# Performance work log

Measured on AMD Instinct MI355X. Metric: run time of the kernel, lower is better.

The kernel has to match this reference:

```python
import jax, jax.numpy as jnp
import numpy as np

N_NODES = 100000
N_EDGES = 1600000
D_IN = 128
D_OUT = 64
NUM_LAYERS = 3
BN_EPS = 1e-5


def setup_inputs() -> dict:
    key = jax.random.key(0)
    k_x, k_e, k_w = jax.random.split(key, 3)
    x = jax.random.normal(k_x, (N_NODES, D_IN), dtype=jnp.float32)
    edge_index = jax.random.randint(k_e, (2, N_EDGES), 0, N_NODES, dtype=jnp.int64)
    bn_gamma = jnp.ones((NUM_LAYERS, D_IN), dtype=jnp.float32)
    bn_beta = jnp.zeros((NUM_LAYERS, D_IN), dtype=jnp.float32)
    W = jax.random.normal(k_w, (D_IN, D_OUT), dtype=jnp.float32) * (1.0 / np.sqrt(D_IN))
    b = jnp.zeros((D_OUT,), dtype=jnp.float32)
    return {"x": x, "edge_index": edge_index, "bn_gamma": bn_gamma, "bn_beta": bn_beta, "W": W, "b": b}


def reference(x, edge_index, bn_gamma, bn_beta, W, b):
    # GNN forward, task='node', aggregate='sum', combine='sum', readout='sum',
    # recursive_weighting=False, training mode (no sigmoid, BN uses batch stats).
    n = x.shape[0]
    dst = edge_index[0]  # spmm(Adj, h): pooled[i] = sum over edges (i <- j) of h[j]
    src = edge_index[1]
    h = x
    for layer in range(NUM_LAYERS):
        # neighbor aggregate: sparse spmm == gather + segment-sum scatter
        agg = jax.ops.segment_sum(h[src], dst, num_segments=n)  # [N, D]
        # graph readout (single batched graph): sum over nodes, broadcast to every node
        readout = jnp.sum(h, axis=0, keepdims=True)  # [1, D]
        # functional 'sum' combine of (self, aggregated, readout)
        h = h + agg + readout
        # BatchNorm1d over the node dimension (training statistics, biased var)
        mean = jnp.mean(h, axis=0)
        var = jnp.var(h, axis=0)
        h = (h - mean) * jax.lax.rsqrt(var + BN_EPS) * bn_gamma[layer] + bn_beta[layer]
        h = jax.nn.relu(h)
    # node-task head (training branch: raw logits)
    return h @ W + b
```

## Files before the change

kernel.cpp:

```cpp
#include <hip/hip_runtime.h>

#define D 128
#define DOUT 64
#define BN_EPS 1e-5f
#define BCAP 96
#define SCAP 224

typedef unsigned int   u32;
typedef unsigned short u16;
typedef short  short8 __attribute__((ext_vector_type(8)));
typedef float  f32x4  __attribute__((ext_vector_type(4)));

__device__ __forceinline__ u16 f2bf(float f) {
    u32 x = __float_as_uint(f);
    x += 0x7fffu + ((x >> 16) & 1u);
    return (u16)(x >> 16);
}
__device__ __forceinline__ float bflo(u32 u) { return __uint_as_float(u << 16); }
__device__ __forceinline__ float bfhi(u32 u) { return __uint_as_float(u & 0xffff0000u); }

__global__ void init_kernel(const float* __restrict__ x, u16* __restrict__ xb,
                            int* __restrict__ bcnt,
                            float* __restrict__ stats,
                            const float* __restrict__ W, u16* __restrict__ wt,
                            int n_nodes, int n_ctr) {
    int total = n_nodes * (D / 4);
    for (int t = blockIdx.x * blockDim.x + threadIdx.x; t < total;
         t += gridDim.x * blockDim.x) {
        float4 v = ((const float4*)x)[t];
        ((ushort4*)xb)[t] = make_ushort4(f2bf(v.x), f2bf(v.y), f2bf(v.z), f2bf(v.w));
        if (t < n_ctr) bcnt[t] = 0;
        if (t < 2048) stats[t] = (t >= 256 && t < 384) ? 1.f : 0.f;
        if (t < D * DOUT) {
            int c = t >> 7, k = t & (D - 1);
            wt[t] = f2bf(W[k * DOUT + c]);
        }
    }
}

__global__ void partA_kernel(const int* __restrict__ ei, int* __restrict__ bcnt,
                             uint2* __restrict__ pairs, int n_edges) {
    int slot = blockIdx.x & 7;
    for (int e = blockIdx.x * blockDim.x + threadIdx.x; e < n_edges;
         e += gridDim.x * blockDim.x) {
        int d = ei[e];
        int s = ei[n_edges + e];
        int sb = ((d >> 6) << 3) + slot;
        int pos = atomicAdd(&bcnt[sb << 4], 1);
        if (pos < SCAP) pairs[(size_t)sb * SCAP + pos] = make_uint2((u32)d, (u32)s);
    }
}

__global__ void partB_kernel(const uint2* __restrict__ pairs,
                             const int* __restrict__ bcnt,
                             int* __restrict__ deg, int* __restrict__ srcs,
                             int n_nodes) {
    __shared__ uint2 lp[8 * SCAP];
    __shared__ int   lsrc[8 * SCAP];
    __shared__ int   cnt[64], st[64], cur[64];
    __shared__ int   sofs[9];
    int b = blockIdx.x;
    int node0 = b << 6;
    if (threadIdx.x == 0) {
        int acc = 0;
        for (int x = 0; x < 8; ++x) {
            sofs[x] = acc;
            acc += min(bcnt[((b << 3) + x) << 4], SCAP);
        }
        sofs[8] = acc;
    }
    if (threadIdx.x < 64) cnt[threadIdx.x] = 0;
    __syncthreads();
    for (int x = 0; x < 8; ++x) {
        int c0 = sofs[x], c1 = sofs[x + 1];
        const uint2* src = pairs + (size_t)((b << 3) + x) * SCAP;
        for (int t = threadIdx.x; t < c1 - c0; t += blockDim.x) {
            uint2 pr = src[t];
            lp[c0 + t] = pr;
            atomicAdd(&cnt[pr.x & 63], 1);
        }
    }
    __syncthreads();
    int cntE = sofs[8];
    if (threadIdx.x == 0) {
        int acc = 0;
        for (int i = 0; i < 64; ++i) { st[i] = acc; cur[i] = acc; acc += cnt[i]; }
    }
    __syncthreads();
    for (int t = threadIdx.x; t < cntE; t += blockDim.x) {
        uint2 pr = lp[t];
        int pos = atomicAdd(&cur[pr.x & 63], 1);
        lsrc[pos] = (int)pr.y;
    }
    __syncthreads();
    int grp = threadIdx.x >> 4, lane = threadIdx.x & 15;
    for (int li = grp; li < 64; li += 16) {
        int node = node0 + li;
        if (node < n_nodes) {
            int d = cnt[li], s0 = st[li];
            for (int t = lane; t < d; t += 16) {
                int key = lsrc[s0 + t];
                int rank = 0;
                for (int u = 0; u < d; ++u) {
                    int o = lsrc[s0 + u];
                    rank += (o < key) || (o == key && u < t);
                }
                if (rank < BCAP) srcs[(size_t)node * BCAP + rank] = key;
            }
            if (lane == 0) deg[node] = d;
        }
    }
}

template <bool APPLY>
__global__ void agg_kernel(const u16* __restrict__ h,
                           const int* __restrict__ srcs,
                           const int* __restrict__ deg,
                           const float* __restrict__ stats_prev,
                           u16* __restrict__ vout,
                           int n_nodes) {
    const int lane = threadIdx.x & 15;
    const int grp  = threadIdx.x >> 4;
    const int c    = lane << 3;
    float sc[8], sh[8];
    #pragma unroll
    for (int k = 0; k < 8; ++k) {
        sc[k] = stats_prev[256 + c + k];
        sh[k] = stats_prev[384 + c + k];
    }
    const int stride = gridDim.x * 16;
    float a[8];

#define ACC(u_) do { \
    float f0 = bflo((u_).x), f1 = bfhi((u_).x); \
    float f2 = bflo((u_).y), f3 = bfhi((u_).y); \
    float f4 = bflo((u_).z), f5 = bfhi((u_).z); \
    float f6 = bflo((u_).w), f7 = bfhi((u_).w); \
    if (APPLY) { \
        a[0] += fmaxf(fmaf(f0, sc[0], sh[0]), 0.f); \
        a[1] += fmaxf(fmaf(f1, sc[1], sh[1]), 0.f); \
        a[2] += fmaxf(fmaf(f2, sc[2], sh[2]), 0.f); \
        a[3] += fmaxf(fmaf(f3, sc[3], sh[3]), 0.f); \
        a[4] += fmaxf(fmaf(f4, sc[4], sh[4]), 0.f); \
        a[5] += fmaxf(fmaf(f5, sc[5], sh[5]), 0.f); \
        a[6] += fmaxf(fmaf(f6, sc[6], sh[6]), 0.f); \
        a[7] += fmaxf(fmaf(f7, sc[7], sh[7]), 0.f); \
    } else { \
        a[0] += f0; a[1] += f1; a[2] += f2; a[3] += f3; \
        a[4] += f4; a[5] += f5; a[6] += f6; a[7] += f7; \
    } } while (0)

    for (int i = blockIdx.x * 16 + grp; i < n_nodes; i += stride) {
        int off = i * BCAP;
        int dg  = min(deg[i], BCAP);
        {
            uint4 u = *(const uint4*)(h + ((size_t)i << 7) + c);
            float f0 = bflo(u.x), f1 = bfhi(u.x), f2 = bflo(u.y), f3 = bfhi(u.y);
            float f4 = bflo(u.z), f5 = bfhi(u.z), f6 = bflo(u.w), f7 = bfhi(u.w);
            float ff[8] = {f0, f1, f2, f3, f4, f5, f6, f7};
            #pragma unroll
            for (int k = 0; k < 8; ++k)
                a[k] = APPLY ? fmaxf(fmaf(ff[k], sc[k], sh[k]), 0.f) : ff[k];
        }
        for (int base = 0; base < dg; base += 16) {
            int cnt = min(dg - base, 16);
            int sv = (lane < cnt) ? srcs[off + base + lane] : 0;
            int k = 0;
            for (; k + 4 <= cnt; k += 4) {
                int j0 = __shfl(sv, k + 0, 16), j1 = __shfl(sv, k + 1, 16);
                int j2 = __shfl(sv, k + 2, 16), j3 = __shfl(sv, k + 3, 16);
                uint4 b0 = *(const uint4*)(h + ((size_t)j0 << 7) + c);
                uint4 b1 = *(const uint4*)(h + ((size_t)j1 << 7) + c);
                uint4 b2 = *(const uint4*)(h + ((size_t)j2 << 7) + c);
                uint4 b3 = *(const uint4*)(h + ((size_t)j3 << 7) + c);
                ACC(b0); ACC(b1); ACC(b2); ACC(b3);
            }
            for (; k < cnt; ++k) {
                int j0 = __shfl(sv, k, 16);
                uint4 b0 = *(const uint4*)(h + ((size_t)j0 << 7) + c);
                ACC(b0);
            }
        }
        uint4 w;
        w.x = (u32)f2bf(a[0]) | ((u32)f2bf(a[1]) << 16);
        w.y = (u32)f2bf(a[2]) | ((u32)f2bf(a[3]) << 16);
        w.z = (u32)f2bf(a[4]) | ((u32)f2bf(a[5]) << 16);
        w.w = (u32)f2bf(a[6]) | ((u32)f2bf(a[7]) << 16);
        *(uint4*)(vout + ((size_t)i << 7) + c) = w;
    }
#undef ACC
}

__global__ void stats_kernel(const u16* __restrict__ v,
                             float* __restrict__ stats_cur, int n_nodes) {
    int col = threadIdx.x & 63;
    int sub = threadIdx.x >> 6;
    float s1a = 0.f, s1b = 0.f, s2a = 0.f, s2b = 0.f;
    const u32* vp = (const u32*)v;
    for (int r = blockIdx.x * 4 + sub; r < n_nodes; r += gridDim.x * 4) {
        u32 w = vp[(size_t)r * 64 + col];
        float fa = bflo(w), fb = bfhi(w);
        s1a += fa; s1b += fb; s2a += fa * fa; s2b += fb * fb;
    }
    __shared__ float red[4][64][4];
    red[sub][col][0] = s1a; red[sub][col][1] = s1b;
    red[sub][col][2] = s2a; red[sub][col][3] = s2b;
    __syncthreads();
    if (sub == 0) {
        #pragma unroll
        for (int m = 1; m < 4; ++m) {
            red[0][col][0] += red[m][col][0];
            red[0][col][1] += red[m][col][1];
            red[0][col][2] += red[m][col][2];
            red[0][col][3] += red[m][col][3];
        }
        unsafeAtomicAdd(&stats_cur[2 * col + 0], red[0][col][0]);
        unsafeAtomicAdd(&stats_cur[2 * col + 1], red[0][col][1]);
        unsafeAtomicAdd(&stats_cur[128 + 2 * col + 0], red[0][col][2]);
        unsafeAtomicAdd(&stats_cur[128 + 2 * col + 1], red[0][col][3]);
    }
}

__global__ void finalize_stats_kernel(float* __restrict__ stats_cur,
                                      const float* __restrict__ gamma,
                                      const float* __restrict__ beta,
                                      int layer, float inv_n) {
    int f = threadIdx.x;
    float mean = stats_cur[f] * inv_n;
    float var  = stats_cur[128 + f] * inv_n - mean * mean;
    var = fmaxf(var, 0.f);
    float s = gamma[layer * D + f] * rsqrtf(var + BN_EPS);
    stats_cur[256 + f] = s;
    stats_cur[384 + f] = beta[layer * D + f] - mean * s;
}

__global__ __launch_bounds__(256) void head_mfma_kernel(
        const u16* __restrict__ v2, const float* __restrict__ stats3,
        const u16* __restrict__ wt, const float* __restrict__ b,
        float* __restrict__ out, int n_nodes) {
    const int wave = threadIdx.x >> 6;
    const int lane = threadIdx.x & 63;
    const int lo   = lane & 15;
    const int hi   = lane >> 4;

    short8 Bf[4][4];
    #pragma unroll
    for (int ct = 0; ct < 4; ++ct)
        #pragma unroll
        for (int ks = 0; ks < 4; ++ks)
            Bf[ct][ks] = *(const short8*)(wt + (ct * 16 + lo) * D + ks * 32 + hi * 8);

    float sc[4][8], sh[4][8];
    #pragma unroll
    for (int ks = 0; ks < 4; ++ks)
        #pragma unroll
        for (int j = 0; j < 8; ++j) {
            int f = ks * 32 + hi * 8 + j;
            sc[ks][j] = stats3[256 + f];
            sh[ks][j] = stats3[384 + f];
        }
    float bias[4];
    #pragma unroll
    for (int ct = 0; ct < 4; ++ct) bias[ct] = b[ct * 16 + lo];

    const int nrt = (n_nodes + 15) >> 4;
    for (int rt = blockIdx.x * 4 + wave; rt < nrt; rt += gridDim.x * 4) {
        const int r0 = rt << 4;
        const int ar = min(r0 + lo, n_nodes - 1);
        const u16* hrow = v2 + ((size_t)ar << 7);
        f32x4 acc[4];
        #pragma unroll
        for (int ct = 0; ct < 4; ++ct) acc[ct] = (f32x4){0.f, 0.f, 0.f, 0.f};
        #pragma unroll
        for (int ks = 0; ks < 4; ++ks) {
            uint4 u = *(const uint4*)(hrow + ks * 32 + hi * 8);
            float f0 = bflo(u.x), f1 = bfhi(u.x), f2 = bflo(u.y), f3 = bfhi(u.y);
            float f4 = bflo(u.z), f5 = bfhi(u.z), f6 = bflo(u.w), f7 = bfhi(u.w);
            float w0 = fmaxf(fmaf(f0, sc[ks][0], sh[ks][0]), 0.f);
            float w1 = fmaxf(fmaf(f1, sc[ks][1], sh[ks][1]), 0.f);
            float w2 = fmaxf(fmaf(f2, sc[ks][2], sh[ks][2]), 0.f);
            float w3 = fmaxf(fmaf(f3, sc[ks][3], sh[ks][3]), 0.f);
            float w4 = fmaxf(fmaf(f4, sc[ks][4], sh[ks][4]), 0.f);
            float w5 = fmaxf(fmaf(f5, sc[ks][5], sh[ks][5]), 0.f);
            float w6 = fmaxf(fmaf(f6, sc[ks][6], sh[ks][6]), 0.f);
            float w7 = fmaxf(fmaf(f7, sc[ks][7], sh[ks][7]), 0.f);
            union { uint4 u4; short8 s8; } af;
            af.u4.x = (u32)f2bf(w0) | ((u32)f2bf(w1) << 16);
            af.u4.y = (u32)f2bf(w2) | ((u32)f2bf(w3) << 16);
            af.u4.z = (u32)f2bf(w4) | ((u32)f2bf(w5) << 16);
            af.u4.w = (u32)f2bf(w6) | ((u32)f2bf(w7) << 16);
            #pragma unroll
            for (int ct = 0; ct < 4; ++ct)
                acc[ct] = __builtin_amdgcn_mfma_f32_16x16x32_bf16(
                    af.s8, Bf[ct][ks], acc[ct], 0, 0, 0);
        }
        #pragma unroll
        for (int ct = 0; ct < 4; ++ct)
            #pragma unroll
            for (int rg = 0; rg < 4; ++rg) {
                int r = r0 + hi * 4 + rg;
                if (r < n_nodes)
                    out[(size_t)r * DOUT + ct * 16 + lo] = acc[ct][rg] + bias[ct];
            }
    }
}

extern "C" void kernel_launch(void* const* d_in, const int* in_sizes, int n_in,
                              void* d_out, int out_size, void* d_ws, size_t ws_size,
                              hipStream_t stream) {
    const float* x     = (const float*)d_in[0];
    const int*   ei    = (const int*)d_in[1];
    const float* gamma = (const float*)d_in[2];
    const float* beta  = (const float*)d_in[3];
    const float* W     = (const float*)d_in[4];
    const float* bvec  = (const float*)d_in[5];
    float* out = (float*)d_out;

    const int n_nodes = in_sizes[0] / D;
    const int n_edges = in_sizes[1] / 2;
    const int n_bkt   = (n_nodes + 63) >> 6;
    const int n_ctr   = n_bkt * 8 * 16;

    const size_t row_bytes = (size_t)n_nodes * D * sizeof(u16);
    char* p = (char*)d_ws;
    u16*   xb     = (u16*)p;   p += row_bytes;
    u16*   vA     = (u16*)p;   p += row_bytes;
    u16*   vB     = (u16*)p;   p += row_bytes;
    int*   srcs   = (int*)p;   p += (size_t)n_nodes * BCAP * sizeof(int);
    int*   deg    = (int*)p;   p += (size_t)n_nodes * sizeof(int);
    int*   bcnt   = (int*)p;   p += (size_t)n_ctr * sizeof(int);
    float* stats  = (float*)p;
    u16*   Wt     = (u16*)(p + 2048 * sizeof(float));
    uint2* pairs  = (uint2*)vB;

    const float inv_n = 1.0f / (float)n_nodes;

    init_kernel<<<2048, 256, 0, stream>>>(x, xb, bcnt, stats, W, Wt, n_nodes, n_ctr);
    partA_kernel<<<1024, 256, 0, stream>>>(ei, bcnt, pairs, n_edges);
    partB_kernel<<<n_bkt, 256, 0, stream>>>(pairs, bcnt, deg, srcs, n_nodes);

    const u16* h = xb;
    u16* vout = vA;
    for (int L = 0; L < 3; ++L) {
        float* scur = stats + (size_t)(L + 1) * 512;
        const float* sprev = stats + (size_t)L * 512;
        if (L == 0)
            agg_kernel<false><<<4096, 256, 0, stream>>>(h, srcs, deg,
                sprev, vout, n_nodes);
        else
            agg_kernel<true><<<4096, 256, 0, stream>>>(h, srcs, deg,
                sprev, vout, n_nodes);
        stats_kernel<<<512, 256, 0, stream>>>(vout, scur, n_nodes);
        finalize_stats_kernel<<<1, D, 0, stream>>>(scur, gamma, beta, L, inv_n);
        h = vout;
        vout = (vout == vA) ? vB : vA;
    }

    head_mfma_kernel<<<782, 256, 0, stream>>>(h, stats + 3 * 512, Wt, bvec,
                                              out, n_nodes);
}
```

Baseline: 519.7 us.

## Block-local counting sort in edge partitioning with coarser buckets and packed pairs

```diff
diff --git a/kernel.cpp b/kernel.cpp
--- a/kernel.cpp
+++ b/kernel.cpp
@@ -4,7 +4,11 @@
 #define DOUT 64
 #define BN_EPS 1e-5f
 #define BCAP 96
-#define SCAP 224
+
+#define NBK_SHIFT 8
+#define NBK_MAX   512
+#define SLOT_CAP  704
+#define PA_E      4000
 
 typedef unsigned int   u32;
 typedef unsigned short u16;
@@ -38,76 +42,124 @@
     }
 }
 
-__global__ void partA_kernel(const int* __restrict__ ei, int* __restrict__ bcnt,
-                             uint2* __restrict__ pairs, int n_edges) {
-    int slot = blockIdx.x & 7;
-    for (int e = blockIdx.x * blockDim.x + threadIdx.x; e < n_edges;
-         e += gridDim.x * blockDim.x) {
+__global__ __launch_bounds__(256) void partA_kernel(const int* __restrict__ ei,
+                             int* __restrict__ bcnt,
+                             u32* __restrict__ pairs, int n_edges, int n_bkt) {
+    __shared__ u32 ord[PA_E];
+    __shared__ u16 obkt[PA_E];
+    __shared__ int hist[NBK_MAX];
+    __shared__ int scanA[NBK_MAX], scanB[NBK_MAX];
+    __shared__ int st[NBK_MAX], cur[NBK_MAX], gbase[NBK_MAX];
+
+    const int tid  = threadIdx.x;
+    const int slot = blockIdx.x & 7;
+    const int e0   = blockIdx.x * PA_E;
+    const int e1   = min(e0 + PA_E, n_edges);
+
+    for (int i = tid; i < NBK_MAX; i += 256) hist[i] = 0;
+    __syncthreads();
+    for (int e = e0 + tid; e < e1; e += 256)
+        atomicAdd(&hist[ei[e] >> NBK_SHIFT], 1);
+    __syncthreads();
+    for (int i = tid; i < NBK_MAX; i += 256) scanA[i] = hist[i];
+    __syncthreads();
+    int* a = scanA; int* b = scanB;
+    for (int s = 1; s < NBK_MAX; s <<= 1) {
+        for (int i = tid; i < NBK_MAX; i += 256)
+            b[i] = a[i] + (i >= s ? a[i - s] : 0);
+        __syncthreads();
+        int* t_ = a; a = b; b = t_;
+    }
+    for (int x = tid; x < n_bkt; x += 256) {
+        int c   = hist[x];
+        int stx = a[x] - c;
+        st[x] = stx; cur[x] = stx;
+        gbase[x] = c ? atomicAdd(&bcnt[((x << 3) + slot) << 4], c) : 0;
+    }
+    __syncthreads();
+    for (int e = e0 + tid; e < e1; e += 256) {
         int d = ei[e];
         int s = ei[n_edges + e];
-        int sb = ((d >> 6) << 3) + slot;
-        int pos = atomicAdd(&bcnt[sb << 4], 1);
-        if (pos < SCAP) pairs[(size_t)sb * SCAP + pos] = make_uint2((u32)d, (u32)s);
-    }
-}
-
-__global__ void partB_kernel(const uint2* __restrict__ pairs,
+        int x = d >> NBK_SHIFT;
+        int pos = atomicAdd(&cur[x], 1);
+        ord[pos]  = ((u32)(d & 255) << 17) | (u32)s;
+        obkt[pos] = (u16)x;
+    }
+    __syncthreads();
+    const int cntE = e1 - e0;
+    for (int i = tid; i < cntE; i += 256) {
+        int x   = obkt[i];
+        int pos = gbase[x] + (i - st[x]);
+        if (pos < SLOT_CAP)
+            pairs[(size_t)((x << 3) + slot) * SLOT_CAP + pos] = ord[i];
+    }
+}
+
+__global__ __launch_bounds__(256) void partB_kernel(const u32* __restrict__ pairs,
                              const int* __restrict__ bcnt,
                              int* __restrict__ deg, int* __restrict__ srcs,
                              int n_nodes) {
-    __shared__ uint2 lp[8 * SCAP];
-    __shared__ int   lsrc[8 * SCAP];
-    __shared__ int   cnt[64], st[64], cur[64];
-    __shared__ int   sofs[9];
+    __shared__ u32 lp[8 * SLOT_CAP];
+    __shared__ int lsrc[8 * SLOT_CAP];
+    __shared__ int cnt[256], st[256], cur[256];
+    __shared__ int scanA[256], scanB[256];
+    __shared__ int sofs[9];
+    const int tid = threadIdx.x;
     int b = blockIdx.x;
-    int node0 = b << 6;
-    if (threadIdx.x == 0) {
+    int node0 = b << NBK_SHIFT;
+    if (tid == 0) {
         int acc = 0;
         for (int x = 0; x < 8; ++x) {
             sofs[x] = acc;
-            acc += min(bcnt[((b << 3) + x) << 4], SCAP);
+            acc += min(bcnt[((b << 3) + x) << 4], SLOT_CAP);
         }
         sofs[8] = acc;
     }
-    if (threadIdx.x < 64) cnt[threadIdx.x] = 0;
+    cnt[tid] = 0;
     __syncthreads();
     for (int x = 0; x < 8; ++x) {
         int c0 = sofs[x], c1 = sofs[x + 1];
-        const uint2* src = pairs + (size_t)((b << 3) + x) * SCAP;
-        for (int t = threadIdx.x; t < c1 - c0; t += blockDim.x) {
-            uint2 pr = src[t];
+        const u32* src = pairs + (size_t)((b << 3) + x) * SLOT_CAP;
+        for (int t = tid; t < c1 - c0; t += blockDim.x) {
+            u32 pr = src[t];
             lp[c0 + t] = pr;
-            atomicAdd(&cnt[pr.x & 63], 1);
-        }
-    }
+            atomicAdd(&cnt[pr >> 17], 1);
+        }
+    }
+    __syncthreads();
+    scanA[tid] = cnt[tid];
+    __syncthreads();
+    int* a = scanA; int* bb = scanB;
+    for (int s = 1; s < 256; s <<= 1) {
+        bb[tid] = a[tid] + (tid >= s ? a[tid - s] : 0);
+        __syncthreads();
+        int* t_ = a; a = bb; bb = t_;
+    }
+    st[tid] = a[tid] - cnt[tid];
+    cur[tid] = st[tid];
     __syncthreads();
     int cntE = sofs[8];
-    if (threadIdx.x == 0) {
-        int acc = 0;
-        for (int i = 0; i < 64; ++i) { st[i] = acc; cur[i] = acc; acc += cnt[i]; }
-    }
-    __syncthreads();
-    for (int t = threadIdx.x; t < cntE; t += blockDim.x) {
-        uint2 pr = lp[t];
-        int pos = atomicAdd(&cur[pr.x & 63], 1);
-        lsrc[pos] = (int)pr.y;
-    }
-    __syncthreads();
-    int grp = threadIdx.x >> 4, lane = threadIdx.x & 15;
-    for (int li = grp; li < 64; li += 16) {
+    for (int t = tid; t < cntE; t += blockDim.x) {
+        u32 pr = lp[t];
+        int pos = atomicAdd(&cur[pr >> 17], 1);
+        lsrc[pos] = (int)(pr & 0x1FFFFu);
+    }
+    __syncthreads();
+    int grp = tid >> 4, lane = tid & 15;
+    for (int li = grp; li < 256; li += 16) {
         int node = node0 + li;
         if (node < n_nodes) {
-            int d = cnt[li], s0 = st[li];
-            for (int t = lane; t < d; t += 16) {
+            int dg = cnt[li], s0 = st[li];
+            for (int t = lane; t < dg; t += 16) {
                 int key = lsrc[s0 + t];
                 int rank = 0;
-                for (int u = 0; u < d; ++u) {
+                for (int u = 0; u < dg; ++u) {
                     int o = lsrc[s0 + u];
                     rank += (o < key) || (o == key && u < t);
                 }
                 if (rank < BCAP) srcs[(size_t)node * BCAP + rank] = key;
             }
-            if (lane == 0) deg[node] = d;
+            if (lane == 0) deg[node] = dg;
         }
     }
 }
@@ -318,7 +370,7 @@
 
     const int n_nodes = in_sizes[0] / D;
     const int n_edges = in_sizes[1] / 2;
-    const int n_bkt   = (n_nodes + 63) >> 6;
+    const int n_bkt   = (n_nodes + 255) >> 8;
     const int n_ctr   = n_bkt * 8 * 16;
 
     const size_t row_bytes = (size_t)n_nodes * D * sizeof(u16);
@@ -331,12 +383,13 @@
     int*   bcnt   = (int*)p;   p += (size_t)n_ctr * sizeof(int);
     float* stats  = (float*)p;
     u16*   Wt     = (u16*)(p + 2048 * sizeof(float));
-    uint2* pairs  = (uint2*)vB;
+    u32* pairs  = (u32*)vB;
 
     const float inv_n = 1.0f / (float)n_nodes;
 
     init_kernel<<<2048, 256, 0, stream>>>(x, xb, bcnt, stats, W, Wt, n_nodes, n_ctr);
-    partA_kernel<<<1024, 256, 0, stream>>>(ei, bcnt, pairs, n_edges);
+    int pa_grid = ((n_edges + PA_E - 1) / PA_E + 7) & ~7;
+    partA_kernel<<<pa_grid, 256, 0, stream>>>(ei, bcnt, pairs, n_edges, n_bkt);
     partB_kernel<<<n_bkt, 256, 0, stream>>>(pairs, bcnt, deg, srcs, n_nodes);
 
     const u16* h = xb;
```

Measured after the change: 501.4 us. 1.04x faster.
